# Kernel optimization log

Hardware: AMD Instinct MI355X
Metric: run time of the kernel (lower is better)

The kernel has to match this reference:

```python
import jax, jax.numpy as jnp
import numpy as np

HIDDEN = 1024
HEADS = 16
HEAD_DIM = HIDDEN // HEADS
SCALE = HEAD_DIM ** (-0.5)


def setup_inputs() -> dict:
    key = jax.random.key(0)
    ks = jax.random.split(key, 5)
    B, N, C = 8, 1024, HIDDEN
    x = jax.random.normal(ks[0], (B, N, C), dtype=jnp.float32)
    # torch nn.Linear params: weight [out, in], bias [out]
    w_in = jax.random.normal(ks[1], (3 * C, C), dtype=jnp.float32) * (C ** -0.5)
    b_in = jax.random.normal(ks[2], (3 * C,), dtype=jnp.float32) * 0.02
    w_out = jax.random.normal(ks[3], (C, C), dtype=jnp.float32) * (C ** -0.5)
    b_out = jax.random.normal(ks[4], (C,), dtype=jnp.float32) * 0.02
    return {"x": x, "w_in": w_in, "b_in": b_in, "w_out": w_out, "b_out": b_out}


def reference(x, w_in, b_in, w_out, b_out):
    B, N, C = x.shape
    H, D = HEADS, HEAD_DIM
    # in_proj: [B,N,3C] -> (3,B,H,N,D)
    qkv = x @ w_in.T + b_in
    qkv = qkv.reshape(B, N, 3, H, D).transpose(2, 0, 3, 1, 4)
    q, k, v = qkv[0], qkv[1], qkv[2]
    # attention scores scaled after QK^T (same math as scaling q)
    attn = jnp.einsum("bhnd,bhmd->bhnm", q, k) * SCALE
    attn = jax.nn.softmax(attn, axis=-1)
    out = jnp.einsum("bhnm,bhmd->bhnd", attn, v)  # [B,H,N,D]
    out = out.transpose(0, 2, 1, 3).reshape(B, N, C)
    return out @ w_out.T + b_out
```

## Files before the change

kernel.cpp:

```cpp
#include <hip/hip_runtime.h>


typedef __attribute__((ext_vector_type(8))) __bf16 bf16x8;
typedef __attribute__((ext_vector_type(4))) __bf16 bf16x4;
typedef __attribute__((ext_vector_type(4))) float f32x4;
typedef __attribute__((ext_vector_type(4))) short short4v;

__device__ __forceinline__ f32x4 mfma16(bf16x8 a, bf16x8 b, f32x4 c) {
  return __builtin_amdgcn_mfma_f32_16x16x32_bf16(a, b, c, 0, 0, 0);
}

#if __has_builtin(__builtin_amdgcn_mfma_f32_16x16x16bf16_1k)
__device__ __forceinline__ f32x4 mfma_pv(bf16x4 a, bf16x4 b, f32x4 c) {
  short4v as = __builtin_bit_cast(short4v, a);
  short4v bs = __builtin_bit_cast(short4v, b);
  return __builtin_amdgcn_mfma_f32_16x16x16bf16_1k(as, bs, c, 0, 0, 0);
}
#else
__device__ __forceinline__ f32x4 mfma_pv(bf16x4 a, bf16x4 b, f32x4 c) {
  __bf16 z = (__bf16)0.f;
  bf16x8 a8 = {a[0], a[1], a[2], a[3], z, z, z, z};
  bf16x8 b8 = {b[0], b[1], b[2], b[3], z, z, z, z};
  return mfma16(a8, b8, c);
}
#endif

__device__ __forceinline__ float fexp2(float x) {
#if __has_builtin(__builtin_amdgcn_exp2f)
  return __builtin_amdgcn_exp2f(x);
#else
  return exp2f(x);
#endif
}

typedef __attribute__((address_space(1))) const unsigned int gu32;
typedef __attribute__((address_space(3))) unsigned int lu32;

__device__ __forceinline__ void async16(const void* g, void* l) {
  __builtin_amdgcn_global_load_lds((gu32*)g, (lu32*)l, 16, 0, 0);
}

__global__ __launch_bounds__(256) void cvt_all(const float* __restrict__ x,
                                               __bf16* __restrict__ xb,
                                               const float* __restrict__ wi,
                                               __bf16* __restrict__ wib,
                                               const float* __restrict__ wo,
                                               __bf16* __restrict__ wob) {
  int blk = blockIdx.x;
  const float* in;
  __bf16* out;
  int base;
  if (blk < 4096)      { in = x;  out = xb;  base = 0; }
  else if (blk < 5632) { in = wi; out = wib; base = 4096; }
  else                 { in = wo; out = wob; base = 5632; }
  int i = ((blk - base) * 256 + threadIdx.x) * 8;
  float4 a = *(const float4*)(in + i);
  float4 b = *(const float4*)(in + i + 4);
  bf16x8 o;
  o[0] = (__bf16)a.x; o[1] = (__bf16)a.y; o[2] = (__bf16)a.z; o[3] = (__bf16)a.w;
  o[4] = (__bf16)b.x; o[5] = (__bf16)b.y; o[6] = (__bf16)b.z; o[7] = (__bf16)b.w;
  *(bf16x8*)(out + i) = o;
}

template <bool WRITE_VT>
__global__ __launch_bounds__(512, 2) void gemm256(const __bf16* __restrict__ A,
                                                  const __bf16* __restrict__ Bm,
                                                  const float* __restrict__ bias,
                                                  __bf16* __restrict__ C,
                                                  __bf16* __restrict__ vt) {
  __shared__ char lds[131072];
  const int t = threadIdx.x;
  const int wv = t >> 6, lane = t & 63;
  const int q16 = lane & 15, quad = lane >> 4;
  const int wm = wv >> 2, wn = wv & 3;

  const int bid = blockIdx.x;
  const int swz = (bid & 7) * 48 + (bid >> 3);
  const long m0 = (long)(swz & 31) * 256;
  const long n0 = (long)(swz >> 5) * 256;

  const int sr = t >> 3;
  const int sgc = (t & 7) ^ (sr & 7);
  const int ldst = wv * 1024;

  f32x4 zero = {0.f, 0.f, 0.f, 0.f};
  f32x4 acc[8][4];
#pragma unroll
  for (int i = 0; i < 8; ++i)
#pragma unroll
    for (int j = 0; j < 4; ++j) acc[i][j] = zero;

  {
    char* A0 = lds;
    char* B0 = lds + 32768;
#pragma unroll
    for (int i = 0; i < 4; ++i) {
      async16(A + (m0 + i * 64 + sr) * 1024 + sgc * 8, A0 + i * 8192 + ldst);
      async16(Bm + (n0 + i * 64 + sr) * 1024 + sgc * 8, B0 + i * 8192 + ldst);
    }
  }
  asm volatile("s_waitcnt vmcnt(0)" ::);
  __builtin_amdgcn_s_barrier();

  int cur = 0;
#pragma unroll 1
  for (int kt = 0; kt < 1024; kt += 64) {
    const bool pref = kt < 960;
    char* Ac = lds + cur * 65536;
    char* Bc = Ac + 32768;
    char* An = lds + (cur ^ 1) * 65536;
    char* Bn = An + 32768;
    const int ktn = kt + 64;

    bf16x8 bfr[4];
#pragma unroll
    for (int kk = 0; kk < 2; ++kk) {
#pragma unroll
      for (int mh = 0; mh < 2; ++mh) {
        bf16x8 af[4];
#pragma unroll
        for (int mi = 0; mi < 4; ++mi) {
          int ra = wm * 128 + (mh * 4 + mi) * 16 + q16;
          af[mi] = *(const bf16x8*)(Ac + ra * 128 + (((kk * 4 + quad) ^ (ra & 7)) * 16));
        }
        if (mh == 0) {
#pragma unroll
          for (int nj = 0; nj < 4; ++nj) {
            int rb = wn * 64 + nj * 16 + q16;
            bfr[nj] = *(const bf16x8*)(Bc + rb * 128 + (((kk * 4 + quad) ^ (rb & 7)) * 16));
          }
        }
        if (pref && kk == 0) {
          const int i0 = mh * 2, i1 = mh * 2 + 1;
          async16(A + (m0 + i0 * 64 + sr) * 1024 + ktn + sgc * 8, An + i0 * 8192 + ldst);
          async16(A + (m0 + i1 * 64 + sr) * 1024 + ktn + sgc * 8, An + i1 * 8192 + ldst);
          async16(Bm + (n0 + i0 * 64 + sr) * 1024 + ktn + sgc * 8, Bn + i0 * 8192 + ldst);
          async16(Bm + (n0 + i1 * 64 + sr) * 1024 + ktn + sgc * 8, Bn + i1 * 8192 + ldst);
        }
        __builtin_amdgcn_s_barrier();
        __builtin_amdgcn_s_setprio(1);
#pragma unroll
        for (int mi = 0; mi < 4; ++mi)
#pragma unroll
          for (int nj = 0; nj < 4; ++nj)
            acc[mh * 4 + mi][nj] = mfma16(af[mi], bfr[nj], acc[mh * 4 + mi][nj]);
        __builtin_amdgcn_s_setprio(0);
        __builtin_amdgcn_s_barrier();
      }
    }
    if (pref) {
      asm volatile("s_waitcnt vmcnt(0)" ::);
      __builtin_amdgcn_sched_barrier(0);
    }
    __builtin_amdgcn_s_barrier();
    cur ^= 1;
  }

  if (WRITE_VT && n0 >= 2048) {
    const int b = (int)(m0 >> 10);
    const int nbase = (int)(m0 & 1023) + wm * 128;
#pragma unroll
    for (int nj = 0; nj < 4; ++nj) {
      int col = (int)n0 + wn * 64 + nj * 16 + q16;
      int cc = col - 2048;
      int h = cc >> 6, d = cc & 63;
      float bs = bias[col];
      __bf16* vrow = vt + (((long)(b * 16 + h)) << 16) + (long)d * 1024;
#pragma unroll
      for (int mi = 0; mi < 8; ++mi) {
        int n = nbase + mi * 16 + quad * 4;
        bf16x4 o;
#pragma unroll
        for (int r = 0; r < 4; ++r) o[r] = (__bf16)(acc[mi][nj][r] + bs);
        *(bf16x4*)(vrow + n) = o;
      }
    }
  } else {
#pragma unroll
    for (int nj = 0; nj < 4; ++nj) {
      long col = n0 + wn * 64 + nj * 16 + q16;
      float bs = bias[col];
#pragma unroll
      for (int mi = 0; mi < 8; ++mi) {
        long rowb = m0 + wm * 128 + mi * 16 + quad * 4;
#pragma unroll
        for (int r = 0; r < 4; ++r) {
          float v = acc[mi][nj][r] + bs;
          C[(rowb + r) * 3072 + col] = (__bf16)v;
        }
      }
    }
  }
}

template <typename OutT>
__global__ __launch_bounds__(256) void gemm_nt64(const __bf16* __restrict__ A,
                                                 const __bf16* __restrict__ Bm,
                                                 const float* __restrict__ bias,
                                                 OutT* __restrict__ C, int K, int ldc) {
  __shared__ __bf16 As[64 * 64];
  __shared__ __bf16 Bs[128 * 64];
  const int t = threadIdx.x;
  const int wv = t >> 6, lane = t & 63;
  const int q16 = lane & 15, quad = lane >> 4;
  const int wm = wv >> 1, wn = wv & 1;
  const long m0 = (long)blockIdx.x * 64;
  const long n0 = (long)blockIdx.y * 128;

  f32x4 zero = {0.f, 0.f, 0.f, 0.f};
  f32x4 acc[2][4];
#pragma unroll
  for (int i = 0; i < 2; ++i)
#pragma unroll
    for (int j = 0; j < 4; ++j) acc[i][j] = zero;

  char* AsB = (char*)As;
  char* BsB = (char*)Bs;
  const int sr = t >> 3;
  const int gc = (t & 7) ^ (sr & 7);

  for (int kt = 0; kt < K; kt += 64) {
    __syncthreads();
#pragma unroll
    for (int i = 0; i < 2; ++i)
      async16(A + (m0 + i * 32 + sr) * K + kt + gc * 8, AsB + i * 4096 + wv * 1024);
#pragma unroll
    for (int i = 0; i < 4; ++i)
      async16(Bm + (n0 + i * 32 + sr) * K + kt + gc * 8, BsB + i * 4096 + wv * 1024);
    __syncthreads();

#pragma unroll
    for (int kk = 0; kk < 2; ++kk) {
      bf16x8 af[2], bf[4];
#pragma unroll
      for (int i = 0; i < 2; ++i) {
        int ra = wm * 32 + i * 16 + q16;
        af[i] = *(const bf16x8*)(AsB + ra * 128 + (((kk * 4 + quad) ^ (ra & 7)) * 16));
      }
#pragma unroll
      for (int j = 0; j < 4; ++j) {
        int rb = wn * 64 + j * 16 + q16;
        bf[j] = *(const bf16x8*)(BsB + rb * 128 + (((kk * 4 + quad) ^ (rb & 7)) * 16));
      }
#pragma unroll
      for (int i = 0; i < 2; ++i)
#pragma unroll
        for (int j = 0; j < 4; ++j) acc[i][j] = mfma16(af[i], bf[j], acc[i][j]);
    }
  }

#pragma unroll
  for (int j = 0; j < 4; ++j) {
    long col = n0 + wn * 64 + j * 16 + q16;
    float bs = bias[col];
#pragma unroll
    for (int i = 0; i < 2; ++i) {
      long rowb = m0 + wm * 32 + i * 16 + quad * 4;
#pragma unroll
      for (int r = 0; r < 4; ++r) {
        float v = acc[i][j][r] + bs;
        C[(rowb + r) * (long)ldc + col] = (OutT)v;
      }
    }
  }
}

__global__ __launch_bounds__(256) void attn_kernel(const __bf16* __restrict__ qkv,
                                                   const __bf16* __restrict__ vt,
                                                   __bf16* __restrict__ ao) {
  __shared__ __bf16 Ks[64 * 64];
  __shared__ __bf16 Vt[64 * 64];
  const int t = threadIdx.x;
  const int wv = t >> 6, lane = t & 63;
  const int q16 = lane & 15, quad = lane >> 4;
  const int bh = blockIdx.x;
  const int b = bh >> 4, h = bh & 15;
  const int q0 = blockIdx.y * 64;
  const long rowbase = (long)b * 1024;

  bf16x8 qf0, qf1;
  {
    long qrow = rowbase + q0 + wv * 16 + q16;
    const __bf16* qp = qkv + qrow * 3072 + h * 64 + quad * 8;
    qf0 = *(const bf16x8*)qp;
    qf1 = *(const bf16x8*)(qp + 32);
#pragma unroll
    for (int j = 0; j < 8; ++j) {
      qf0[j] = (__bf16)((float)qf0[j] * 0.18033688f);
      qf1[j] = (__bf16)((float)qf1[j] * 0.18033688f);
    }
  }

  f32x4 zero = {0.f, 0.f, 0.f, 0.f};
  f32x4 oacc[4];
#pragma unroll
  for (int dt = 0; dt < 4; ++dt) oacc[dt] = zero;
  float lcol = 0.f;

  char* KsB = (char*)Ks;
  char* VtB = (char*)Vt;
  const int sr = t >> 3;
  const int sgc = (t & 7) ^ (sr & 7);
  const int sw = q16 & 7;

  for (int kv0 = 0; kv0 < 1024; kv0 += 64) {
    __syncthreads();
    const __bf16* kg = qkv + (rowbase + kv0 + sr) * 3072 + 1024 + h * 64 + sgc * 8;
    async16(kg, KsB + wv * 1024);
    async16(kg + (long)32 * 3072, KsB + 4096 + wv * 1024);
    const __bf16* vg = vt + (long)bh * 65536 + (long)sr * 1024 + kv0 + sgc * 8;
    async16(vg, VtB + wv * 1024);
    async16(vg + (long)32 * 1024, VtB + 4096 + wv * 1024);
    __syncthreads();

    f32x4 sacc[4];
#pragma unroll
    for (int nt = 0; nt < 4; ++nt) sacc[nt] = zero;
#pragma unroll
    for (int nt = 0; nt < 4; ++nt) {
      int kvr = nt * 16 + q16;
      bf16x8 kf0 = *(const bf16x8*)(KsB + kvr * 128 + ((quad ^ sw) * 16));
      bf16x8 kf1 = *(const bf16x8*)(KsB + kvr * 128 + (((4 + quad) ^ sw) * 16));
      sacc[nt] = mfma16(kf0, qf0, sacc[nt]);
      sacc[nt] = mfma16(kf1, qf1, sacc[nt]);
    }

    bf16x4 pf[4];
#pragma unroll
    for (int nt = 0; nt < 4; ++nt)
#pragma unroll
      for (int r = 0; r < 4; ++r) {
        float p = fexp2(sacc[nt][r]);
        lcol += p;
        pf[nt][r] = (__bf16)p;
      }

#pragma unroll
    for (int nt = 0; nt < 4; ++nt) {
      int c = ((nt * 2 + (quad >> 1)) ^ sw) * 16 + (quad & 1) * 8;
#pragma unroll
      for (int dt = 0; dt < 4; ++dt) {
        bf16x4 vf = *(const bf16x4*)(VtB + (dt * 16 + q16) * 128 + c);
        oacc[dt] = mfma_pv(pf[nt], vf, oacc[dt]);
      }
    }
  }

  lcol += __shfl_xor(lcol, 16);
  lcol += __shfl_xor(lcol, 32);
  float inv = 1.0f / lcol;
#pragma unroll
  for (int r = 0; r < 4; ++r) {
    float ir = __shfl(inv, quad * 4 + r);
    long orow = rowbase + q0 + wv * 16 + quad * 4 + r;
#pragma unroll
    for (int dt = 0; dt < 4; ++dt)
      ao[orow * 1024 + h * 64 + dt * 16 + q16] = (__bf16)(oacc[dt][r] * ir);
  }
}

extern "C" void kernel_launch(void* const* d_in, const int* in_sizes, int n_in,
                              void* d_out, int out_size, void* d_ws, size_t ws_size,
                              hipStream_t stream) {
  const float* x     = (const float*)d_in[0];
  const float* w_in  = (const float*)d_in[1];
  const float* b_in  = (const float*)d_in[2];
  const float* w_out = (const float*)d_in[3];
  const float* b_out = (const float*)d_in[4];
  float* out = (float*)d_out;

  char* ws = (char*)d_ws;
  __bf16* xb   = (__bf16*)(ws);
  __bf16* wib  = (__bf16*)(ws + 16777216);
  __bf16* wob  = (__bf16*)(ws + 23068672);
  __bf16* qkvb = (__bf16*)(ws + 25165824);
  __bf16* aob  = (__bf16*)(ws + 75497472);
  __bf16* vtg  = (__bf16*)d_out;

  cvt_all<<<6144, 256, 0, stream>>>(x, xb, w_in, wib, w_out, wob);
  gemm256<true><<<384, 512, 0, stream>>>(xb, wib, b_in, qkvb, vtg);
  attn_kernel<<<dim3(128, 16), 256, 0, stream>>>(qkvb, vtg, aob);
  gemm_nt64<float><<<dim3(128, 8), 256, 0, stream>>>(
      aob, wob, b_out, out, 1024, 1024);
}
```

Baseline: 248.0 us.

## Restructure QKV GEMM to 256x128 tiles with 3-stage K32 LDS pipeline

Replaces the 256x256 double-buffered K64 QKV projection GEMM with a 256x128 tile kernel using a triple-buffered K=32 LDS ring and vmcnt-based waits, doubling the grid to 768 blocks. Each wave now owns a 64x64 sub-tile with fewer accumulators, LDS shrinks to 72KB, and launch bounds ask for 4 waves per SIMD. The aim is more in-flight loads and better CU fill at the cost of more B-tile reloads and the loss of the block-index swizzle for L2 locality.

After: 234.7 us. 5.4% less time.

```diff
diff --git a/kernel.cpp b/kernel.cpp
--- a/kernel.cpp
+++ b/kernel.cpp
@@ -63,102 +63,97 @@
 }
 
 template <bool WRITE_VT>
-__global__ __launch_bounds__(512, 2) void gemm256(const __bf16* __restrict__ A,
-                                                  const __bf16* __restrict__ Bm,
-                                                  const float* __restrict__ bias,
-                                                  __bf16* __restrict__ C,
-                                                  __bf16* __restrict__ vt) {
-  __shared__ char lds[131072];
+__global__ __launch_bounds__(512, 4) void gemm1(const __bf16* __restrict__ A,
+                                                const __bf16* __restrict__ Bm,
+                                                const float* __restrict__ bias,
+                                                __bf16* __restrict__ C,
+                                                __bf16* __restrict__ vt) {
+  __shared__ char lds[73728];
   const int t = threadIdx.x;
   const int wv = t >> 6, lane = t & 63;
   const int q16 = lane & 15, quad = lane >> 4;
-  const int wm = wv >> 2, wn = wv & 3;
-
+  const int wm = wv >> 1, wn = wv & 1;
   const int bid = blockIdx.x;
-  const int swz = (bid & 7) * 48 + (bid >> 3);
-  const long m0 = (long)(swz & 31) * 256;
-  const long n0 = (long)(swz >> 5) * 256;
-
-  const int sr = t >> 3;
-  const int sgc = (t & 7) ^ (sr & 7);
+  const long m0 = (long)(bid & 31) * 256;
+  const long n0 = (long)(bid >> 5) * 128;
+
+  const int sr4 = t >> 2;
+  const int gc = (t & 3) ^ ((sr4 >> 2) & 3);
   const int ldst = wv * 1024;
 
+  const __bf16* srcA0 = A + (m0 + sr4) * 1024 + gc * 8;
+  const __bf16* srcA1 = A + (m0 + 128 + sr4) * 1024 + gc * 8;
+  const __bf16* srcB  = Bm + (n0 + sr4) * 1024 + gc * 8;
+
+  const int raB = (wm * 64 + q16) * 64 + ((quad ^ (q16 >> 2)) * 16);
+  const int rbB = (wn * 64 + q16) * 64 + ((quad ^ (q16 >> 2)) * 16);
+
   f32x4 zero = {0.f, 0.f, 0.f, 0.f};
-  f32x4 acc[8][4];
-#pragma unroll
-  for (int i = 0; i < 8; ++i)
+  f32x4 acc[4][4];
+#pragma unroll
+  for (int i = 0; i < 4; ++i)
 #pragma unroll
     for (int j = 0; j < 4; ++j) acc[i][j] = zero;
 
   {
-    char* A0 = lds;
-    char* B0 = lds + 32768;
-#pragma unroll
-    for (int i = 0; i < 4; ++i) {
-      async16(A + (m0 + i * 64 + sr) * 1024 + sgc * 8, A0 + i * 8192 + ldst);
-      async16(Bm + (n0 + i * 64 + sr) * 1024 + sgc * 8, B0 + i * 8192 + ldst);
-    }
-  }
-  asm volatile("s_waitcnt vmcnt(0)" ::);
+    char* b0 = lds;
+    async16(srcA0, b0 + ldst);
+    async16(srcA1, b0 + 8192 + ldst);
+    async16(srcB, b0 + 16384 + ldst);
+    char* b1 = lds + 24576;
+    async16(srcA0 + 32, b1 + ldst);
+    async16(srcA1 + 32, b1 + 8192 + ldst);
+    async16(srcB + 32, b1 + 16384 + ldst);
+  }
+  asm volatile("s_waitcnt vmcnt(3)" ::);
   __builtin_amdgcn_s_barrier();
 
-  int cur = 0;
+  int bread = 0;
 #pragma unroll 1
-  for (int kt = 0; kt < 1024; kt += 64) {
-    const bool pref = kt < 960;
-    char* Ac = lds + cur * 65536;
-    char* Bc = Ac + 32768;
-    char* An = lds + (cur ^ 1) * 65536;
-    char* Bn = An + 32768;
-    const int ktn = kt + 64;
-
-    bf16x8 bfr[4];
-#pragma unroll
-    for (int kk = 0; kk < 2; ++kk) {
-#pragma unroll
-      for (int mh = 0; mh < 2; ++mh) {
-        bf16x8 af[4];
-#pragma unroll
-        for (int mi = 0; mi < 4; ++mi) {
-          int ra = wm * 128 + (mh * 4 + mi) * 16 + q16;
-          af[mi] = *(const bf16x8*)(Ac + ra * 128 + (((kk * 4 + quad) ^ (ra & 7)) * 16));
-        }
-        if (mh == 0) {
-#pragma unroll
-          for (int nj = 0; nj < 4; ++nj) {
-            int rb = wn * 64 + nj * 16 + q16;
-            bfr[nj] = *(const bf16x8*)(Bc + rb * 128 + (((kk * 4 + quad) ^ (rb & 7)) * 16));
-          }
-        }
-        if (pref && kk == 0) {
-          const int i0 = mh * 2, i1 = mh * 2 + 1;
-          async16(A + (m0 + i0 * 64 + sr) * 1024 + ktn + sgc * 8, An + i0 * 8192 + ldst);
-          async16(A + (m0 + i1 * 64 + sr) * 1024 + ktn + sgc * 8, An + i1 * 8192 + ldst);
-          async16(Bm + (n0 + i0 * 64 + sr) * 1024 + ktn + sgc * 8, Bn + i0 * 8192 + ldst);
-          async16(Bm + (n0 + i1 * 64 + sr) * 1024 + ktn + sgc * 8, Bn + i1 * 8192 + ldst);
-        }
-        __builtin_amdgcn_s_barrier();
-        __builtin_amdgcn_s_setprio(1);
-#pragma unroll
-        for (int mi = 0; mi < 4; ++mi)
-#pragma unroll
-          for (int nj = 0; nj < 4; ++nj)
-            acc[mh * 4 + mi][nj] = mfma16(af[mi], bfr[nj], acc[mh * 4 + mi][nj]);
-        __builtin_amdgcn_s_setprio(0);
-        __builtin_amdgcn_s_barrier();
-      }
-    }
-    if (pref) {
+  for (int t32 = 0; t32 < 32; ++t32) {
+    char* Ac = lds + bread * 24576;
+    char* Bc = Ac + 16384;
+
+    if (t32 < 30) {
+      int bst = bread + 2;
+      if (bst >= 3) bst -= 3;
+      char* S = lds + bst * 24576;
+      const int kt = (t32 + 2) * 32;
+      async16(srcA0 + kt, S + ldst);
+      async16(srcA1 + kt, S + 8192 + ldst);
+      async16(srcB + kt, S + 16384 + ldst);
+    }
+
+    bf16x8 af[4], bfr[4];
+#pragma unroll
+    for (int mi = 0; mi < 4; ++mi)
+      af[mi] = *(const bf16x8*)(Ac + raB + mi * 1024);
+#pragma unroll
+    for (int nj = 0; nj < 4; ++nj)
+      bfr[nj] = *(const bf16x8*)(Bc + rbB + nj * 1024);
+
+    __builtin_amdgcn_s_barrier();
+    __builtin_amdgcn_s_setprio(1);
+#pragma unroll
+    for (int mi = 0; mi < 4; ++mi)
+#pragma unroll
+      for (int nj = 0; nj < 4; ++nj)
+        acc[mi][nj] = mfma16(af[mi], bfr[nj], acc[mi][nj]);
+    __builtin_amdgcn_s_setprio(0);
+
+    if (t32 < 30) {
+      asm volatile("s_waitcnt vmcnt(3)" ::);
+    } else if (t32 == 30) {
       asm volatile("s_waitcnt vmcnt(0)" ::);
-      __builtin_amdgcn_sched_barrier(0);
     }
     __builtin_amdgcn_s_barrier();
-    cur ^= 1;
+    bread = bread + 1;
+    if (bread >= 3) bread -= 3;
   }
 
   if (WRITE_VT && n0 >= 2048) {
     const int b = (int)(m0 >> 10);
-    const int nbase = (int)(m0 & 1023) + wm * 128;
+    const int nbase = (int)(m0 & 1023) + wm * 64;
 #pragma unroll
     for (int nj = 0; nj < 4; ++nj) {
       int col = (int)n0 + wn * 64 + nj * 16 + q16;
@@ -167,7 +162,7 @@
       float bs = bias[col];
       __bf16* vrow = vt + (((long)(b * 16 + h)) << 16) + (long)d * 1024;
 #pragma unroll
-      for (int mi = 0; mi < 8; ++mi) {
+      for (int mi = 0; mi < 4; ++mi) {
         int n = nbase + mi * 16 + quad * 4;
         bf16x4 o;
 #pragma unroll
@@ -181,8 +176,8 @@
       long col = n0 + wn * 64 + nj * 16 + q16;
       float bs = bias[col];
 #pragma unroll
-      for (int mi = 0; mi < 8; ++mi) {
-        long rowb = m0 + wm * 128 + mi * 16 + quad * 4;
+      for (int mi = 0; mi < 4; ++mi) {
+        long rowb = m0 + wm * 64 + mi * 16 + quad * 4;
 #pragma unroll
         for (int r = 0; r < 4; ++r) {
           float v = acc[mi][nj][r] + bs;
@@ -378,7 +373,7 @@
   __bf16* vtg  = (__bf16*)d_out;
 
   cvt_all<<<6144, 256, 0, stream>>>(x, xb, w_in, wib, w_out, wob);
-  gemm256<true><<<384, 512, 0, stream>>>(xb, wib, b_in, qkvb, vtg);
+  gemm1<true><<<768, 512, 0, stream>>>(xb, wib, b_in, qkvb, vtg);
   attn_kernel<<<dim3(128, 16), 256, 0, stream>>>(qkvb, vtg, aob);
   gemm_nt64<float><<<dim3(128, 8), 256, 0, stream>>>(
       aob, wob, b_out, out, 1024, 1024);
```
